# Kernel optimization log

Hardware: AMD Instinct MI355X
Metric: run time of the kernel (lower is better)

Reference implementation:

```python
import jax, jax.numpy as jnp
import numpy as np

# dims
L, D, N, H, FF, F = 2, 512, 8, 64, 2048, 256   # layers, embed, heads, head_dim, ffn, feature_dim
BQ, BC, TQ, TC = 8, 32, 128, 128               # query batch, candidate batch, tokens
EPS = 1e-6


def setup_inputs() -> dict:
    key = jax.random.key(0)
    ks = iter(jax.random.split(key, 64))
    nrm = lambda shape, s=0.02: jax.random.normal(next(ks), shape, jnp.float32) * s
    inp = {
        "c": jax.random.normal(next(ks), (BC, TC, D), jnp.float32),
        "q": jax.random.normal(next(ks), (BQ, TQ, D), jnp.float32),
    }
    for p in ("sa", "ca"):  # self-attn / cross-attn per decoder layer, stacked over L
        inp[f"{p}_wq"] = nrm((L, D, N, H)); inp[f"{p}_bq"] = nrm((L, N, 1, H))
        inp[f"{p}_wk"] = nrm((L, D, N, H)); inp[f"{p}_bk"] = nrm((L, N, 1, H))
        inp[f"{p}_wv"] = nrm((L, D, N, H)); inp[f"{p}_bv"] = nrm((L, N, 1, H))
        inp[f"{p}_wo"] = nrm((L, N, D, H)); inp[f"{p}_bo"] = nrm((L, D))
    for i in (1, 2, 3):  # post-norm LayerNorms
        inp[f"ln{i}_g"] = jnp.ones((L, D), jnp.float32)
        inp[f"ln{i}_b"] = jnp.zeros((L, D), jnp.float32)
    inp["ffn_w1"] = nrm((L, D, FF)); inp["ffn_b1"] = jnp.zeros((L, FF), jnp.float32)
    inp["ffn_w2"] = nrm((L, FF, D)); inp["ffn_b2"] = jnp.zeros((L, D), jnp.float32)
    inp["lnf_g"] = jnp.ones((D,), jnp.float32); inp["lnf_b"] = jnp.zeros((D,), jnp.float32)
    inp["feat_wq"] = nrm((D, F)); inp["feat_bq"] = jnp.zeros((F,), jnp.float32)
    inp["feat_wc"] = nrm((D, F)); inp["feat_bc"] = jnp.zeros((F,), jnp.float32)
    return inp


def _ln(x, g, b):
    m = x.mean(-1, keepdims=True)
    v = ((x - m) ** 2).mean(-1, keepdims=True)
    return (x - m) * jax.lax.rsqrt(v + EPS) * g + b


def _mha4d(xq, xkv, wq, bq, wk, bk, wv, bv, wo, bo):
    # query reads axes as (e,b), key/value as (b,e): the swapped leading axes make
    # the matmul broadcast queries against candidates when e/b are singleton.
    Q = jnp.einsum('ebtd,dnh->ebnth', xq, wq) + bq   # [e,b,n,t,h]
    K = jnp.einsum('betd,dnh->benth', xkv, wk) + bk  # [b,e,n,s,h]
    V = jnp.einsum('betd,dnh->benth', xkv, wv) + bv
    scores = jnp.matmul(Q, jnp.swapaxes(K, -1, -2)) / np.sqrt(H)  # broadcast -> [B,E,n,t,s]
    A = jax.nn.softmax(scores, axis=-1)
    O = jnp.matmul(A, V)                              # [B,E,n,t,h]
    return jnp.einsum('benth,ndh->betd', O, wo) + bo  # [B,E,t,d]


def reference(c, q, sa_wq, sa_bq, sa_wk, sa_bk, sa_wv, sa_bv, sa_wo, sa_bo,
              ca_wq, ca_bq, ca_wk, ca_bk, ca_wv, ca_bv, ca_wo, ca_bo,
              ln1_g, ln1_b, ln2_g, ln2_b, ln3_g, ln3_b,
              ffn_w1, ffn_b1, ffn_w2, ffn_b2, lnf_g, lnf_b,
              feat_wq, feat_bq, feat_wc, feat_bc):
    qm = q[:, None]   # [BQ,1,TQ,D]  encoder memory
    x = c[None]       # [1,BC,TC,D]  decoder input
    for i in range(L):
        a = _mha4d(x, x, sa_wq[i], sa_bq[i], sa_wk[i], sa_bk[i], sa_wv[i], sa_bv[i], sa_wo[i], sa_bo[i])
        x = _ln(x + a, ln1_g[i], ln1_b[i])
        a = _mha4d(x, qm, ca_wq[i], ca_bq[i], ca_wk[i], ca_bk[i], ca_wv[i], ca_bv[i], ca_wo[i], ca_bo[i])
        x = _ln(x + a, ln2_g[i], ln2_b[i])  # x: [BQ,BC,TC,D]
        h = jax.nn.relu(x @ ffn_w1[i] + ffn_b1[i]) @ ffn_w2[i] + ffn_b2[i]
        x = _ln(x + h, ln3_g[i], ln3_b[i])
    x = _ln(x, lnf_g, lnf_b)
    # pooling='avg': drop token 0 then mean over token axis (axis=2)
    qp = qm[:, :, 1:, :].mean(axis=2)  # [BQ,1,D]
    cp = x[:, :, 1:, :].mean(axis=2)   # [BQ,BC,D]
    qf = qp @ feat_wq + feat_bq        # [BQ,1,F]
    cf = cp @ feat_wc + feat_bc        # [BQ,BC,F]
    qn = qf * jax.lax.rsqrt(jnp.maximum((qf ** 2).sum(-1, keepdims=True), 1e-12))
    cn = cf * jax.lax.rsqrt(jnp.maximum((cf ** 2).sum(-1, keepdims=True), 1e-12))
    return (qn * cn).sum(-1)           # [BQ,BC] cosine similarity
```

## Files before the change

kernel.cpp:

```cpp
#include <hip/hip_runtime.h>

using half4  = __attribute__((ext_vector_type(4))) _Float16;
using half8  = __attribute__((ext_vector_type(8))) _Float16;
using floatx4 = __attribute__((ext_vector_type(4))) float;

__device__ __forceinline__ void gl_lds16(const _Float16* g, _Float16* l)
{
  __builtin_amdgcn_global_load_lds(
      (const __attribute__((address_space(1))) void*)g,
      (__attribute__((address_space(3))) void*)l, 16, 0, 0);
}

__global__ __launch_bounds__(256) void gemm_h(
    const _Float16* __restrict__ A, const _Float16* __restrict__ Bt,
    const float* __restrict__ bias, _Float16* __restrict__ C,
    int M, int N, int K, int ldC, int relu)
{
  __shared__ _Float16 As[128 * 32];
  __shared__ _Float16 Bs[128 * 32];
  int tid = threadIdx.x;
  int lane = tid & 63, wave = tid >> 6;
  long bm0 = (long)blockIdx.y * 128;
  int bn0 = blockIdx.x * 128;
  int wm = (wave & 1) * 64, wn = (wave >> 1) * 64;
  int srow = wave * 16 + (lane >> 2);
  int scol = (((lane & 3) ^ ((lane >> 3) & 3)) * 8);
  const _Float16* aA0 = A + (bm0 + srow) * (long)K + scol;
  const _Float16* aA1 = aA0 + 64 * (long)K;
  const _Float16* aB0 = Bt + (bn0 + srow) * (long)K + scol;
  const _Float16* aB1 = aB0 + 64 * (long)K;
  _Float16* lA0 = As + wave * 512;
  _Float16* lA1 = As + 2048 + wave * 512;
  _Float16* lB0 = Bs + wave * 512;
  _Float16* lB1 = Bs + 2048 + wave * 512;
  int mrow = lane & 15, quad = lane >> 4;
  int cofs = (quad ^ ((mrow >> 1) & 3)) * 8;
  floatx4 acc[4][4];
#pragma unroll
  for (int i = 0; i < 4; ++i)
#pragma unroll
    for (int j = 0; j < 4; ++j) acc[i][j] = (floatx4){0.f, 0.f, 0.f, 0.f};

  for (int kt = 0; kt < K; kt += 32) {
    __syncthreads();
    gl_lds16(aA0 + kt, lA0);
    gl_lds16(aA1 + kt, lA1);
    gl_lds16(aB0 + kt, lB0);
    gl_lds16(aB1 + kt, lB1);
    __syncthreads();
    half8 af[4], bf[4];
#pragma unroll
    for (int i = 0; i < 4; ++i)
      af[i] = *(const half8*)&As[(wm + 16 * i + mrow) * 32 + cofs];
#pragma unroll
    for (int j = 0; j < 4; ++j)
      bf[j] = *(const half8*)&Bs[(wn + 16 * j + mrow) * 32 + cofs];
#pragma unroll
    for (int i = 0; i < 4; ++i)
#pragma unroll
      for (int j = 0; j < 4; ++j)
        acc[i][j] = __builtin_amdgcn_mfma_f32_16x16x32_f16(af[i], bf[j], acc[i][j], 0, 0, 0);
  }
#pragma unroll
  for (int j = 0; j < 4; ++j) {
    int n = bn0 + wn + 16 * j + mrow;
    float bj = bias[n];
#pragma unroll
    for (int i = 0; i < 4; ++i) {
#pragma unroll
      for (int r = 0; r < 4; ++r) {
        long m = bm0 + wm + 16 * i + quad * 4 + r;
        float v = acc[i][j][r] + bj;
        if (relu) v = fmaxf(v, 0.f);
        C[m * (long)ldC + n] = (_Float16)v;
      }
    }
  }
}

__global__ __launch_bounds__(256, 2) void gemm_2(
    const _Float16* __restrict__ A, const _Float16* __restrict__ Bt,
    const float* __restrict__ bias, _Float16* __restrict__ C,
    int MT, int NT, int K, int ldC, int relu)
{
  __shared__ _Float16 As[256 * 64];
  __shared__ _Float16 Bs[128 * 64];
  int tid = threadIdx.x;
  int lane = tid & 63, wave = tid >> 6;
  int L = blockIdx.x;
  int xcd = L & 7, seq = L >> 3;
  int band = MT >> 3;
  int mt = xcd * band + seq / NT;
  int nt = seq - (seq / NT) * NT;
  long bm0 = (long)mt * 256;
  int bn0 = nt * 128;
  int r8 = lane >> 3, s8 = lane & 7;
  int scol = (s8 ^ r8) * 8;
  const _Float16* aA = A + (bm0 + wave * 64 + r8) * (long)K + scol;
  const _Float16* aB = Bt + (bn0 + wave * 32 + r8) * (long)K + scol;
  _Float16* lA = As + (wave * 64) * 64;
  _Float16* lB = Bs + (wave * 32) * 64;
  int ll = lane & 15, quad = lane >> 4;
  int lw = ll & 7;
  floatx4 acc[4][8];
#pragma unroll
  for (int i = 0; i < 4; ++i)
#pragma unroll
    for (int j = 0; j < 8; ++j) acc[i][j] = (floatx4){0.f, 0.f, 0.f, 0.f};

  for (int kt = 0; kt < K; kt += 64) {
    __syncthreads();
#pragma unroll
    for (int o = 0; o < 8; ++o)
      gl_lds16(aA + (long)(o * 8) * K + kt, lA + o * 512);
#pragma unroll
    for (int o = 0; o < 4; ++o)
      gl_lds16(aB + (long)(o * 8) * K + kt, lB + o * 512);
    __syncthreads();
#pragma unroll
    for (int k2 = 0; k2 < 2; ++k2) {
      int sofs = ((k2 * 4 + quad) ^ lw) * 8;
      half8 af[4], bf[8];
#pragma unroll
      for (int i = 0; i < 4; ++i)
        af[i] = *(const half8*)&As[(wave * 64 + 16 * i + ll) * 64 + sofs];
#pragma unroll
      for (int j = 0; j < 8; ++j)
        bf[j] = *(const half8*)&Bs[(16 * j + ll) * 64 + sofs];
#pragma unroll
      for (int i = 0; i < 4; ++i)
#pragma unroll
        for (int j = 0; j < 8; ++j)
          acc[i][j] = __builtin_amdgcn_mfma_f32_16x16x32_f16(af[i], bf[j], acc[i][j], 0, 0, 0);
    }
  }
#pragma unroll
  for (int j = 0; j < 8; ++j) {
    int n = bn0 + 16 * j + ll;
    float bj = bias[n];
#pragma unroll
    for (int i = 0; i < 4; ++i) {
#pragma unroll
      for (int r = 0; r < 4; ++r) {
        long m = bm0 + wave * 64 + 16 * i + quad * 4 + r;
        float v = acc[i][j][r] + bj;
        if (relu) v = fmaxf(v, 0.f);
        C[m * (long)ldC + n] = (_Float16)v;
      }
    }
  }
}

__global__ __launch_bounds__(256) void attn_h(
    const _Float16* __restrict__ Qp, int qs,
    const _Float16* __restrict__ Kp, const _Float16* __restrict__ Vp, int ks,
    _Float16* __restrict__ Op, int mode_ca, int l0, int rb0)
{
  __shared__ _Float16 KV[128 * 72];
  __shared__ _Float16 Ps[128 * 136];
  int tid = threadIdx.x;
  int lane = tid & 63, wave = tid >> 6;
  int ll = lane & 15, quad = lane >> 4;
  int idx = blockIdx.x;
  int n = idx & 7;
  int rl = idx >> 3;
  long obase = (long)rl * 128 * 512 + n * 64;
  long qoff, koff;
  if (!mode_ca) {
    qoff = (long)rl * 128 * qs + n * 64;
    koff = (long)rl * 128 * ks + n * 64;
  } else {
    int g = rb0 + rl;
    int a = g >> 5;
    int qblk = l0 ? (g & 31) : rl;
    qoff = (long)qblk * 128 * qs + n * 64;
    koff = (long)a * 128 * ks + n * 64;
  }
#pragma unroll
  for (int it = 0; it < 4; ++it) {
    int e = tid + it * 256;
    int r = e >> 3, c = (e & 7) * 8;
    *(half8*)&KV[r * 72 + c] = *(const half8*)&Kp[koff + (long)r * ks + c];
  }
  half8 aQ[2][2];
#pragma unroll
  for (int i = 0; i < 2; ++i)
#pragma unroll
    for (int k2 = 0; k2 < 2; ++k2)
      aQ[i][k2] = *(const half8*)&Qp[qoff + (long)(wave * 32 + i * 16 + ll) * qs
                                     + quad * 8 + k2 * 32];
  half8 vreg[4];
#pragma unroll
  for (int it = 0; it < 4; ++it) {
    int e = tid + it * 256;
    int vr = e >> 3, c = (e & 7) * 8;
    vreg[it] = *(const half8*)&Vp[koff + (long)vr * ks + c];
  }
  __syncthreads();
  floatx4 accS[2][8];
#pragma unroll
  for (int i = 0; i < 2; ++i)
#pragma unroll
    for (int j = 0; j < 8; ++j) accS[i][j] = (floatx4){0.f, 0.f, 0.f, 0.f};
#pragma unroll
  for (int k2 = 0; k2 < 2; ++k2) {
#pragma unroll
    for (int j = 0; j < 8; ++j) {
      half8 bK = *(const half8*)&KV[(j * 16 + ll) * 72 + quad * 8 + k2 * 32];
      accS[0][j] = __builtin_amdgcn_mfma_f32_16x16x32_f16(aQ[0][k2], bK, accS[0][j], 0, 0, 0);
      accS[1][j] = __builtin_amdgcn_mfma_f32_16x16x32_f16(aQ[1][k2], bK, accS[1][j], 0, 0, 0);
    }
  }
  float rinv[2][4];
#pragma unroll
  for (int i = 0; i < 2; ++i) {
#pragma unroll
    for (int r = 0; r < 4; ++r) {
      float mx = -1e30f;
#pragma unroll
      for (int j = 0; j < 8; ++j) {
        accS[i][j][r] *= 0.125f;
        mx = fmaxf(mx, accS[i][j][r]);
      }
#pragma unroll
      for (int off = 1; off < 16; off <<= 1) mx = fmaxf(mx, __shfl_xor(mx, off));
      float s = 0.f;
#pragma unroll
      for (int j = 0; j < 8; ++j) {
        float e = __expf(accS[i][j][r] - mx);
        accS[i][j][r] = e;
        s += e;
      }
#pragma unroll
      for (int off = 1; off < 16; off <<= 1) s += __shfl_xor(s, off);
      rinv[i][r] = 1.f / s;
      int prow = wave * 32 + i * 16 + quad * 4 + r;
#pragma unroll
      for (int j = 0; j < 8; ++j)
        Ps[prow * 136 + j * 16 + ll] = (_Float16)accS[i][j][r];
    }
  }
  __syncthreads();
#pragma unroll
  for (int it = 0; it < 4; ++it) {
    int e = tid + it * 256;
    int vr = e >> 3, c = (e & 7) * 8;
#pragma unroll
    for (int j = 0; j < 8; ++j) KV[(c + j) * 132 + vr] = vreg[it][j];
  }
  __syncthreads();
  floatx4 accO[2][4];
#pragma unroll
  for (int i = 0; i < 2; ++i)
#pragma unroll
    for (int j = 0; j < 4; ++j) accO[i][j] = (floatx4){0.f, 0.f, 0.f, 0.f};
#pragma unroll
  for (int k4 = 0; k4 < 4; ++k4) {
    half8 aP[2];
#pragma unroll
    for (int i = 0; i < 2; ++i)
      aP[i] = *(const half8*)&Ps[(wave * 32 + i * 16 + ll) * 136 + quad * 8 + k4 * 32];
#pragma unroll
    for (int jh = 0; jh < 4; ++jh) {
      int vb = (jh * 16 + ll) * 132 + quad * 8 + k4 * 32;
      half4 v0 = *(const half4*)&KV[vb];
      half4 v1 = *(const half4*)&KV[vb + 4];
      half8 bV = __builtin_shufflevector(v0, v1, 0, 1, 2, 3, 4, 5, 6, 7);
      accO[0][jh] = __builtin_amdgcn_mfma_f32_16x16x32_f16(aP[0], bV, accO[0][jh], 0, 0, 0);
      accO[1][jh] = __builtin_amdgcn_mfma_f32_16x16x32_f16(aP[1], bV, accO[1][jh], 0, 0, 0);
    }
  }
#pragma unroll
  for (int i = 0; i < 2; ++i)
#pragma unroll
    for (int jh = 0; jh < 4; ++jh)
#pragma unroll
      for (int r = 0; r < 4; ++r) {
        int m = wave * 32 + i * 16 + quad * 4 + r;
        Op[obase + (long)m * 512 + jh * 16 + ll] = (_Float16)(accO[i][jh][r] * rinv[i][r]);
      }
}

__global__ __launch_bounds__(256) void ln_h(
    const void* __restrict__ xin, int xf32, const _Float16* __restrict__ add,
    _Float16* __restrict__ out, const float* __restrict__ g,
    const float* __restrict__ bt, long row0, int bmask)
{
  int rl = blockIdx.x * 4 + (threadIdx.x >> 6);
  long row = row0 + rl;
  int lane = threadIdx.x & 63;
  long xr = (row & (long)bmask) * 512 + lane * 8;
  float v[8];
  if (xf32) {
    float4 a0 = *(const float4*)((const float*)xin + xr);
    float4 a1 = *(const float4*)((const float*)xin + xr + 4);
    v[0] = a0.x; v[1] = a0.y; v[2] = a0.z; v[3] = a0.w;
    v[4] = a1.x; v[5] = a1.y; v[6] = a1.z; v[7] = a1.w;
  } else {
    half8 h = *(const half8*)((const _Float16*)xin + xr);
#pragma unroll
    for (int i = 0; i < 8; ++i) v[i] = (float)h[i];
  }
  if (add) {
    half8 a = *(const half8*)&add[(long)rl * 512 + lane * 8];
#pragma unroll
    for (int i = 0; i < 8; ++i) v[i] += (float)a[i];
  }
  float s = 0.f, sq = 0.f;
#pragma unroll
  for (int i = 0; i < 8; ++i) { s += v[i]; sq += v[i] * v[i]; }
#pragma unroll
  for (int off = 1; off < 64; off <<= 1) {
    s += __shfl_xor(s, off);
    sq += __shfl_xor(sq, off);
  }
  float mean = s * (1.f / 512.f);
  float var = sq * (1.f / 512.f) - mean * mean;
  float rst = rsqrtf(var + 1e-6f);
  int c = lane * 8;
  float4 g0 = *(const float4*)&g[c], g1 = *(const float4*)&g[c + 4];
  float4 b0 = *(const float4*)&bt[c], b1 = *(const float4*)&bt[c + 4];
  float gg[8] = {g0.x, g0.y, g0.z, g0.w, g1.x, g1.y, g1.z, g1.w};
  float bb[8] = {b0.x, b0.y, b0.z, b0.w, b1.x, b1.y, b1.z, b1.w};
  half8 o;
#pragma unroll
  for (int i = 0; i < 8; ++i) o[i] = (_Float16)((v[i] - mean) * rst * gg[i] + bb[i]);
  *(half8*)&out[row * 512 + c] = o;
}

__global__ __launch_bounds__(256) void tconv512(
    const float* __restrict__ w0, const float* __restrict__ w1,
    const float* __restrict__ w2, const float* __restrict__ w3,
    const float* __restrict__ w4, const float* __restrict__ w5,
    _Float16* __restrict__ Wh)
{
  __shared__ float T[64][65];
  int z = blockIdx.z;
  int t = z >> 1, l = z & 1;
  const float* src;
  long off;
  switch (t) {
    case 0: src = w0; off = 0; break;
    case 1: src = w1; off = 262144; break;
    case 2: src = w2; off = 524288; break;
    case 3: src = w3; off = 1048576; break;
    case 4: src = w4; off = 1310720; break;
    default: src = w5; off = 1572864; break;
  }
  src += (long)l * 262144;
  _Float16* out = Wh + (long)l * 4194304 + off;
  int tx = threadIdx.x & 63, tg = threadIdx.x >> 6;
  int r0 = blockIdx.y * 64, c0 = blockIdx.x * 64;
#pragma unroll
  for (int i = 0; i < 16; ++i)
    T[tg + 4 * i][tx] = src[(long)(r0 + tg + 4 * i) * 512 + c0 + tx];
  __syncthreads();
#pragma unroll
  for (int i = 0; i < 16; ++i)
    out[(long)(c0 + tg + 4 * i) * 512 + r0 + tx] = (_Float16)T[tx][tg + 4 * i];
}

__global__ __launch_bounds__(256) void tconvL(const float* __restrict__ in,
                                              _Float16* __restrict__ out, int Rr, int Cc,
                                              long ils, long ols)
{
  __shared__ float T[64][65];
  in += (long)blockIdx.z * ils;
  out += (long)blockIdx.z * ols;
  int tx = threadIdx.x & 63, tg = threadIdx.x >> 6;
  int r0 = blockIdx.y * 64, c0 = blockIdx.x * 64;
#pragma unroll
  for (int i = 0; i < 16; ++i)
    T[tg + 4 * i][tx] = in[(long)(r0 + tg + 4 * i) * Cc + c0 + tx];
  __syncthreads();
#pragma unroll
  for (int i = 0; i < 16; ++i)
    out[(long)(c0 + tg + 4 * i) * Rr + r0 + tx] = (_Float16)T[tx][tg + 4 * i];
}

__global__ void woconvB(const float* __restrict__ sa_wo, const float* __restrict__ ca_wo,
                        _Float16* __restrict__ Wh)
{
  int z = blockIdx.y;
  int s = z >> 1, l = z & 1;
  const float* wo = (s ? ca_wo : sa_wo) + (long)l * 262144;
  _Float16* out = Wh + (long)l * 4194304 + (s ? 1835008 : 786432);
  int o = blockIdx.x * 256 + threadIdx.x;
  int d = o >> 9;
  int nh = o & 511;
  int n = nh >> 6, h = nh & 63;
  out[o] = (_Float16)wo[((long)(n << 9) + d) * 64 + h];
}

__global__ void packbias(const float* __restrict__ sa_bq, const float* __restrict__ sa_bk,
                         const float* __restrict__ sa_bv, const float* __restrict__ ca_bk,
                         const float* __restrict__ ca_bv, float* __restrict__ Bqkv,
                         float* __restrict__ Bkv)
{
  int i = blockIdx.x * 256 + threadIdx.x;
  if (i >= 5120) return;
  int reg = i >> 9, idx = i & 511;
  int l = reg / 5, r = reg % 5;
  int lo = l * 512;
  switch (r) {
    case 0: Bqkv[l * 1536 + idx] = sa_bq[lo + idx]; break;
    case 1: Bqkv[l * 1536 + 512 + idx] = sa_bk[lo + idx]; break;
    case 2: Bqkv[l * 1536 + 1024 + idx] = sa_bv[lo + idx]; break;
    case 3: Bkv[l * 1024 + idx] = ca_bk[lo + idx]; break;
    default: Bkv[l * 1024 + 512 + idx] = ca_bv[lo + idx]; break;
  }
}

__global__ void f2h2(const float* __restrict__ a, _Float16* __restrict__ oa, long na,
                     const float* __restrict__ bsrc, _Float16* __restrict__ ob, long nb)
{
  long i = blockIdx.x * 256L + threadIdx.x;
  if (i < na) oa[i] = (_Float16)a[i];
  else if (i < na + nb) ob[i - na] = (_Float16)bsrc[i - na];
}

__global__ void featq_pool(const float* __restrict__ q, const float* __restrict__ W,
                           const float* __restrict__ bias, float* __restrict__ QN)
{
  __shared__ float sh[512];
  __shared__ float red[256];
  int a = blockIdx.x;
  int f = threadIdx.x;
  for (int dd = f; dd < 512; dd += 256) {
    const float* base = q + (long)a * 65536 + dd;
    float s = 0.f;
    for (int t = 1; t < 128; ++t) s += base[t * 512];
    sh[dd] = s * (1.f / 127.f);
  }
  __syncthreads();
  float acc = bias[f];
  for (int d = 0; d < 512; ++d) acc += sh[d] * W[d * 256 + f];
  red[f] = acc * acc;
  __syncthreads();
  for (int s = 128; s > 0; s >>= 1) {
    if (f < s) red[f] += red[f + s];
    __syncthreads();
  }
  float rn = rsqrtf(fmaxf(red[0], 1e-12f));
  QN[a * 256 + f] = acc * rn;
}

__global__ void featc_pool(const _Float16* __restrict__ X, const float* __restrict__ W,
                           const float* __restrict__ bias, const float* __restrict__ QN,
                           float* __restrict__ out)
{
  __shared__ float sh[512];
  __shared__ float red[256];
  int ab = blockIdx.x;
  int f = threadIdx.x;
  for (int dd = f; dd < 512; dd += 256) {
    const _Float16* base = X + (long)ab * 65536 + dd;
    float s = 0.f;
    for (int t = 1; t < 128; ++t) s += (float)base[t * 512];
    sh[dd] = s * (1.f / 127.f);
  }
  __syncthreads();
  float acc = bias[f];
  for (int d = 0; d < 512; ++d) acc += sh[d] * W[d * 256 + f];
  red[f] = acc * acc;
  __syncthreads();
  for (int s = 128; s > 0; s >>= 1) {
    if (f < s) red[f] += red[f + s];
    __syncthreads();
  }
  float rn = rsqrtf(fmaxf(red[0], 1e-12f));
  float v = acc * rn * QN[(ab >> 5) * 256 + f];
  __syncthreads();
  red[f] = v;
  __syncthreads();
  for (int s = 128; s > 0; s >>= 1) {
    if (f < s) red[f] += red[f + s];
    __syncthreads();
  }
  if (f == 0) out[ab] = red[0];
}

extern "C" void kernel_launch(void* const* d_in, const int* in_sizes, int n_in,
                              void* d_out, int out_size, void* d_ws, size_t ws_size,
                              hipStream_t stream)
{
  (void)in_sizes; (void)n_in; (void)out_size;
  const float* c_in  = (const float*)d_in[0];
  const float* q_in  = (const float*)d_in[1];
  const float* sa_wq = (const float*)d_in[2];
  const float* sa_bq = (const float*)d_in[3];
  const float* sa_wk = (const float*)d_in[4];
  const float* sa_bk = (const float*)d_in[5];
  const float* sa_wv = (const float*)d_in[6];
  const float* sa_bv = (const float*)d_in[7];
  const float* sa_wo = (const float*)d_in[8];
  const float* sa_bo = (const float*)d_in[9];
  const float* ca_wq = (const float*)d_in[10];
  const float* ca_bq = (const float*)d_in[11];
  const float* ca_wk = (const float*)d_in[12];
  const float* ca_bk = (const float*)d_in[13];
  const float* ca_wv = (const float*)d_in[14];
  const float* ca_bv = (const float*)d_in[15];
  const float* ca_wo = (const float*)d_in[16];
  const float* ca_bo = (const float*)d_in[17];
  const float* ln1_g = (const float*)d_in[18];
  const float* ln1_b = (const float*)d_in[19];
  const float* ln2_g = (const float*)d_in[20];
  const float* ln2_b = (const float*)d_in[21];
  const float* ln3_g = (const float*)d_in[22];
  const float* ln3_b = (const float*)d_in[23];
  const float* ffn_w1 = (const float*)d_in[24];
  const float* ffn_b1 = (const float*)d_in[25];
  const float* ffn_w2 = (const float*)d_in[26];
  const float* ffn_b2 = (const float*)d_in[27];
  const float* lnf_g  = (const float*)d_in[28];
  const float* lnf_b  = (const float*)d_in[29];
  const float* feat_wq = (const float*)d_in[30];
  const float* feat_bq = (const float*)d_in[31];
  const float* feat_wc = (const float*)d_in[32];
  const float* feat_bc = (const float*)d_in[33];

  char* p = (char*)d_ws;
  _Float16* Xh  = (_Float16*)p;  p += 33554432;
  _Float16* Xsh = (_Float16*)p;  p += 4194304;
  _Float16* Wh  = (_Float16*)p;  p += 16777216;
  _Float16* qh  = (_Float16*)p;  p += 1048576;
  _Float16* KV0 = (_Float16*)p;  p += 2097152;
  float*    Bqkv = (float*)p;    p += 12288;
  float*    Bkv  = (float*)p;    p += 8192;
  float*    QN  = (float*)p;     p += 8192;
  const size_t fixed_b = (size_t)(p - (char*)d_ws);
  long R = 4096;
  if (ws_size >= fixed_b + 5120UL * 32768) R = 32768;
  else if (ws_size >= fixed_b + 5120UL * 16384) R = 16384;
  else if (ws_size >= fixed_b + 5120UL * 8192) R = 8192;
  _Float16* QKVc = (_Float16*)p; p += R * 3072;
  _Float16* Oc   = (_Float16*)p; p += R * 1024;
  _Float16* Ac   = (_Float16*)p;
  _Float16* Hb = QKVc;
  const int MTR = (int)(R / 256);

  f2h2<<<10240, 256, 0, stream>>>(c_in, Xsh, 2097152, q_in, qh, 524288);
  tconv512<<<dim3(8, 8, 12), 256, 0, stream>>>(sa_wq, sa_wk, sa_wv, ca_wq, ca_wk, ca_wv, Wh);
  woconvB<<<dim3(1024, 4), 256, 0, stream>>>(sa_wo, ca_wo, Wh);
  tconvL<<<dim3(32, 8, 2), 256, 0, stream>>>(ffn_w1, Wh + 2097152, 512, 2048, 1048576, 4194304);
  tconvL<<<dim3(8, 32, 2), 256, 0, stream>>>(ffn_w2, Wh + 3145728, 2048, 512, 1048576, 4194304);
  packbias<<<20, 256, 0, stream>>>(sa_bq, sa_bk, sa_bv, ca_bk, ca_bv, Bqkv, Bkv);

  {
    _Float16* Wl = Wh;
    gemm_h<<<dim3(12, 32), 256, 0, stream>>>(Xsh, Wl + 0, Bqkv, QKVc, 4096, 1536, 512, 1536, 0);
    attn_h<<<256, 256, 0, stream>>>(QKVc, 1536, QKVc + 512, QKVc + 1024, 1536, Oc, 0, 0, 0);
    gemm_h<<<dim3(4, 32), 256, 0, stream>>>(Oc, Wl + 786432, sa_bo, Ac, 4096, 512, 512, 512, 0);
    ln_h<<<1024, 256, 0, stream>>>(c_in, 1, Ac, Xsh, ln1_g, ln1_b, 0, 0x7FFFFFFF);
    gemm_h<<<dim3(4, 32), 256, 0, stream>>>(Xsh, Wl + 1048576, ca_bq, QKVc, 4096, 512, 512, 1536, 0);
    gemm_h<<<dim3(8, 8), 256, 0, stream>>>(qh, Wl + 1310720, Bkv, KV0, 1024, 1024, 512, 1024, 0);
    for (long c = 0; c < 32768; c += R) {
      attn_h<<<(R / 128) * 8, 256, 0, stream>>>(QKVc, 1536, KV0, KV0 + 512, 1024, Oc,
                                                1, 1, (int)(c / 128));
      gemm_2<<<MTR * 4, 256, 0, stream>>>(Oc, Wl + 1835008, ca_bo, Ac, MTR, 4, 512, 512, 0);
      ln_h<<<R / 4, 256, 0, stream>>>(Xsh, 0, Ac, Xh, ln2_g, ln2_b, c, 4095);
      gemm_2<<<MTR * 16, 256, 0, stream>>>(Xh + c * 512, Wl + 2097152,
                                           ffn_b1, Hb, MTR, 16, 512, 2048, 1);
      gemm_2<<<MTR * 4, 256, 0, stream>>>(Hb, Wl + 3145728, ffn_b2, Ac, MTR, 4, 2048, 512, 0);
      ln_h<<<R / 4, 256, 0, stream>>>(Xh, 0, Ac, Xh, ln3_g, ln3_b, c, 0x7FFFFFFF);
    }
  }
  {
    _Float16* Wl = Wh + 4194304;
    gemm_h<<<dim3(8, 8), 256, 0, stream>>>(qh, Wl + 1310720, Bkv + 1024, KV0, 1024, 1024, 512, 1024, 0);
    for (long c = 0; c < 32768; c += R) {
      _Float16* Xhc = Xh + c * 512;
      gemm_2<<<MTR * 12, 256, 0, stream>>>(Xhc, Wl + 0, Bqkv + 1536, QKVc, MTR, 12, 512, 1536, 0);
      attn_h<<<(R / 128) * 8, 256, 0, stream>>>(QKVc, 1536, QKVc + 512, QKVc + 1024, 1536,
                                                Oc, 0, 0, 0);
      gemm_2<<<MTR * 4, 256, 0, stream>>>(Oc, Wl + 786432, sa_bo + 512, Ac, MTR, 4, 512, 512, 0);
      ln_h<<<R / 4, 256, 0, stream>>>(Xh, 0, Ac, Xh, ln1_g + 512, ln1_b + 512, c, 0x7FFFFFFF);
      gemm_2<<<MTR * 4, 256, 0, stream>>>(Xhc, Wl + 1048576, ca_bq + 512, QKVc, MTR, 4, 512, 1536, 0);
      attn_h<<<(R / 128) * 8, 256, 0, stream>>>(QKVc, 1536, KV0, KV0 + 512, 1024, Oc,
                                                1, 0, (int)(c / 128));
      gemm_2<<<MTR * 4, 256, 0, stream>>>(Oc, Wl + 1835008, ca_bo + 512, Ac, MTR, 4, 512, 512, 0);
      ln_h<<<R / 4, 256, 0, stream>>>(Xh, 0, Ac, Xh, ln2_g + 512, ln2_b + 512, c, 0x7FFFFFFF);
      gemm_2<<<MTR * 16, 256, 0, stream>>>(Xh + c * 512, Wl + 2097152,
                                           ffn_b1 + 2048, Hb, MTR, 16, 512, 2048, 1);
      gemm_2<<<MTR * 4, 256, 0, stream>>>(Hb, Wl + 3145728, ffn_b2 + 512, Ac, MTR, 4, 2048, 512, 0);
      ln_h<<<R / 4, 256, 0, stream>>>(Xh, 0, Ac, Xh, ln3_g + 512, ln3_b + 512, c, 0x7FFFFFFF);
    }
  }
  ln_h<<<8192, 256, 0, stream>>>(Xh, 0, nullptr, Xh, lnf_g, lnf_b, 0, 0x7FFFFFFF);
  featq_pool<<<8, 256, 0, stream>>>(q_in, feat_wq, feat_bq, QN);
  featc_pool<<<256, 256, 0, stream>>>(Xh, feat_wc, feat_bc, QN, (float*)d_out);
}
```

Baseline: 925.7 us.

## Replace 256x128 gemm_2 with 128x128 gemm_h and fuse final LayerNorm

Removes the larger-tile gemm_2 kernel (256x128 tiles, K-step 64, XCD-aware block mapping) and routes every chunked GEMM through the 128x128 gemm_h kernel. Separately, the final LayerNorm is folded into the last layer's ln3 launch through an optional second gamma/beta pair, which drops one full pass over the activations. The smaller tiles give more blocks per launch but lower data reuse per block and lose the XCD-aware scheduling.

Result: slower. 1.156 ms (+24.9%).

```diff
diff --git a/kernel.cpp b/kernel.cpp
--- a/kernel.cpp
+++ b/kernel.cpp
@@ -78,79 +78,6 @@
   }
 }
 
-__global__ __launch_bounds__(256, 2) void gemm_2(
-    const _Float16* __restrict__ A, const _Float16* __restrict__ Bt,
-    const float* __restrict__ bias, _Float16* __restrict__ C,
-    int MT, int NT, int K, int ldC, int relu)
-{
-  __shared__ _Float16 As[256 * 64];
-  __shared__ _Float16 Bs[128 * 64];
-  int tid = threadIdx.x;
-  int lane = tid & 63, wave = tid >> 6;
-  int L = blockIdx.x;
-  int xcd = L & 7, seq = L >> 3;
-  int band = MT >> 3;
-  int mt = xcd * band + seq / NT;
-  int nt = seq - (seq / NT) * NT;
-  long bm0 = (long)mt * 256;
-  int bn0 = nt * 128;
-  int r8 = lane >> 3, s8 = lane & 7;
-  int scol = (s8 ^ r8) * 8;
-  const _Float16* aA = A + (bm0 + wave * 64 + r8) * (long)K + scol;
-  const _Float16* aB = Bt + (bn0 + wave * 32 + r8) * (long)K + scol;
-  _Float16* lA = As + (wave * 64) * 64;
-  _Float16* lB = Bs + (wave * 32) * 64;
-  int ll = lane & 15, quad = lane >> 4;
-  int lw = ll & 7;
-  floatx4 acc[4][8];
-#pragma unroll
-  for (int i = 0; i < 4; ++i)
-#pragma unroll
-    for (int j = 0; j < 8; ++j) acc[i][j] = (floatx4){0.f, 0.f, 0.f, 0.f};
-
-  for (int kt = 0; kt < K; kt += 64) {
-    __syncthreads();
-#pragma unroll
-    for (int o = 0; o < 8; ++o)
-      gl_lds16(aA + (long)(o * 8) * K + kt, lA + o * 512);
-#pragma unroll
-    for (int o = 0; o < 4; ++o)
-      gl_lds16(aB + (long)(o * 8) * K + kt, lB + o * 512);
-    __syncthreads();
-#pragma unroll
-    for (int k2 = 0; k2 < 2; ++k2) {
-      int sofs = ((k2 * 4 + quad) ^ lw) * 8;
-      half8 af[4], bf[8];
-#pragma unroll
-      for (int i = 0; i < 4; ++i)
-        af[i] = *(const half8*)&As[(wave * 64 + 16 * i + ll) * 64 + sofs];
-#pragma unroll
-      for (int j = 0; j < 8; ++j)
-        bf[j] = *(const half8*)&Bs[(16 * j + ll) * 64 + sofs];
-#pragma unroll
-      for (int i = 0; i < 4; ++i)
-#pragma unroll
-        for (int j = 0; j < 8; ++j)
-          acc[i][j] = __builtin_amdgcn_mfma_f32_16x16x32_f16(af[i], bf[j], acc[i][j], 0, 0, 0);
-    }
-  }
-#pragma unroll
-  for (int j = 0; j < 8; ++j) {
-    int n = bn0 + 16 * j + ll;
-    float bj = bias[n];
-#pragma unroll
-    for (int i = 0; i < 4; ++i) {
-#pragma unroll
-      for (int r = 0; r < 4; ++r) {
-        long m = bm0 + wave * 64 + 16 * i + quad * 4 + r;
-        float v = acc[i][j][r] + bj;
-        if (relu) v = fmaxf(v, 0.f);
-        C[m * (long)ldC + n] = (_Float16)v;
-      }
-    }
-  }
-}
-
 __global__ __launch_bounds__(256) void attn_h(
     const _Float16* __restrict__ Qp, int qs,
     const _Float16* __restrict__ Kp, const _Float16* __restrict__ Vp, int ks,
@@ -284,7 +211,8 @@
 __global__ __launch_bounds__(256) void ln_h(
     const void* __restrict__ xin, int xf32, const _Float16* __restrict__ add,
     _Float16* __restrict__ out, const float* __restrict__ g,
-    const float* __restrict__ bt, long row0, int bmask)
+    const float* __restrict__ bt, long row0, int bmask,
+    const float* __restrict__ g2, const float* __restrict__ bt2)
 {
   int rl = blockIdx.x * 4 + (threadIdx.x >> 6);
   long row = row0 + rl;
@@ -322,9 +250,30 @@
   float4 b0 = *(const float4*)&bt[c], b1 = *(const float4*)&bt[c + 4];
   float gg[8] = {g0.x, g0.y, g0.z, g0.w, g1.x, g1.y, g1.z, g1.w};
   float bb[8] = {b0.x, b0.y, b0.z, b0.w, b1.x, b1.y, b1.z, b1.w};
+#pragma unroll
+  for (int i = 0; i < 8; ++i) v[i] = (v[i] - mean) * rst * gg[i] + bb[i];
+  if (g2) {
+    float s2 = 0.f, sq2 = 0.f;
+#pragma unroll
+    for (int i = 0; i < 8; ++i) { s2 += v[i]; sq2 += v[i] * v[i]; }
+#pragma unroll
+    for (int off = 1; off < 64; off <<= 1) {
+      s2 += __shfl_xor(s2, off);
+      sq2 += __shfl_xor(sq2, off);
+    }
+    float mean2 = s2 * (1.f / 512.f);
+    float var2 = sq2 * (1.f / 512.f) - mean2 * mean2;
+    float rst2 = rsqrtf(var2 + 1e-6f);
+    float4 e0 = *(const float4*)&g2[c], e1 = *(const float4*)&g2[c + 4];
+    float4 f0 = *(const float4*)&bt2[c], f1 = *(const float4*)&bt2[c + 4];
+    float ee[8] = {e0.x, e0.y, e0.z, e0.w, e1.x, e1.y, e1.z, e1.w};
+    float ff[8] = {f0.x, f0.y, f0.z, f0.w, f1.x, f1.y, f1.z, f1.w};
+#pragma unroll
+    for (int i = 0; i < 8; ++i) v[i] = (v[i] - mean2) * rst2 * ee[i] + ff[i];
+  }
   half8 o;
 #pragma unroll
-  for (int i = 0; i < 8; ++i) o[i] = (_Float16)((v[i] - mean) * rst * gg[i] + bb[i]);
+  for (int i = 0; i < 8; ++i) o[i] = (_Float16)v[i];
   *(half8*)&out[row * 512 + c] = o;
 }
 
@@ -538,7 +487,7 @@
   _Float16* Oc   = (_Float16*)p; p += R * 1024;
   _Float16* Ac   = (_Float16*)p;
   _Float16* Hb = QKVc;
-  const int MTR = (int)(R / 256);
+  const int MR = (int)(R / 128);
 
   f2h2<<<10240, 256, 0, stream>>>(c_in, Xsh, 2097152, q_in, qh, 524288);
   tconv512<<<dim3(8, 8, 12), 256, 0, stream>>>(sa_wq, sa_wk, sa_wv, ca_wq, ca_wk, ca_wv, Wh);
@@ -552,18 +501,23 @@
     gemm_h<<<dim3(12, 32), 256, 0, stream>>>(Xsh, Wl + 0, Bqkv, QKVc, 4096, 1536, 512, 1536, 0);
     attn_h<<<256, 256, 0, stream>>>(QKVc, 1536, QKVc + 512, QKVc + 1024, 1536, Oc, 0, 0, 0);
     gemm_h<<<dim3(4, 32), 256, 0, stream>>>(Oc, Wl + 786432, sa_bo, Ac, 4096, 512, 512, 512, 0);
-    ln_h<<<1024, 256, 0, stream>>>(c_in, 1, Ac, Xsh, ln1_g, ln1_b, 0, 0x7FFFFFFF);
+    ln_h<<<1024, 256, 0, stream>>>(c_in, 1, Ac, Xsh, ln1_g, ln1_b, 0, 0x7FFFFFFF,
+                                   nullptr, nullptr);
     gemm_h<<<dim3(4, 32), 256, 0, stream>>>(Xsh, Wl + 1048576, ca_bq, QKVc, 4096, 512, 512, 1536, 0);
     gemm_h<<<dim3(8, 8), 256, 0, stream>>>(qh, Wl + 1310720, Bkv, KV0, 1024, 1024, 512, 1024, 0);
     for (long c = 0; c < 32768; c += R) {
       attn_h<<<(R / 128) * 8, 256, 0, stream>>>(QKVc, 1536, KV0, KV0 + 512, 1024, Oc,
                                                 1, 1, (int)(c / 128));
-      gemm_2<<<MTR * 4, 256, 0, stream>>>(Oc, Wl + 1835008, ca_bo, Ac, MTR, 4, 512, 512, 0);
-      ln_h<<<R / 4, 256, 0, stream>>>(Xsh, 0, Ac, Xh, ln2_g, ln2_b, c, 4095);
-      gemm_2<<<MTR * 16, 256, 0, stream>>>(Xh + c * 512, Wl + 2097152,
-                                           ffn_b1, Hb, MTR, 16, 512, 2048, 1);
-      gemm_2<<<MTR * 4, 256, 0, stream>>>(Hb, Wl + 3145728, ffn_b2, Ac, MTR, 4, 2048, 512, 0);
-      ln_h<<<R / 4, 256, 0, stream>>>(Xh, 0, Ac, Xh, ln3_g, ln3_b, c, 0x7FFFFFFF);
+      gemm_h<<<dim3(4, MR), 256, 0, stream>>>(Oc, Wl + 1835008, ca_bo, Ac,
+                                              (int)R, 512, 512, 512, 0);
+      ln_h<<<R / 4, 256, 0, stream>>>(Xsh, 0, Ac, Xh, ln2_g, ln2_b, c, 4095,
+                                      nullptr, nullptr);
+      gemm_h<<<dim3(16, MR), 256, 0, stream>>>(Xh + c * 512, Wl + 2097152,
+                                               ffn_b1, Hb, (int)R, 2048, 512, 2048, 1);
+      gemm_h<<<dim3(4, MR), 256, 0, stream>>>(Hb, Wl + 3145728, ffn_b2, Ac,
+                                              (int)R, 512, 2048, 512, 0);
+      ln_h<<<R / 4, 256, 0, stream>>>(Xh, 0, Ac, Xh, ln3_g, ln3_b, c, 0x7FFFFFFF,
+                                      nullptr, nullptr);
     }
   }
   {
@@ -571,23 +525,30 @@
     gemm_h<<<dim3(8, 8), 256, 0, stream>>>(qh, Wl + 1310720, Bkv + 1024, KV0, 1024, 1024, 512, 1024, 0);
     for (long c = 0; c < 32768; c += R) {
       _Float16* Xhc = Xh + c * 512;
-      gemm_2<<<MTR * 12, 256, 0, stream>>>(Xhc, Wl + 0, Bqkv + 1536, QKVc, MTR, 12, 512, 1536, 0);
+      gemm_h<<<dim3(12, MR), 256, 0, stream>>>(Xhc, Wl + 0, Bqkv + 1536, QKVc,
+                                               (int)R, 1536, 512, 1536, 0);
       attn_h<<<(R / 128) * 8, 256, 0, stream>>>(QKVc, 1536, QKVc + 512, QKVc + 1024, 1536,
                                                 Oc, 0, 0, 0);
-      gemm_2<<<MTR * 4, 256, 0, stream>>>(Oc, Wl + 786432, sa_bo + 512, Ac, MTR, 4, 512, 512, 0);
-      ln_h<<<R / 4, 256, 0, stream>>>(Xh, 0, Ac, Xh, ln1_g + 512, ln1_b + 512, c, 0x7FFFFFFF);
-      gemm_2<<<MTR * 4, 256, 0, stream>>>(Xhc, Wl + 1048576, ca_bq + 512, QKVc, MTR, 4, 512, 1536, 0);
+      gemm_h<<<dim3(4, MR), 256, 0, stream>>>(Oc, Wl + 786432, sa_bo + 512, Ac,
+                                              (int)R, 512, 512, 512, 0);
+      ln_h<<<R / 4, 256, 0, stream>>>(Xh, 0, Ac, Xh, ln1_g + 512, ln1_b + 512, c, 0x7FFFFFFF,
+                                      nullptr, nullptr);
+      gemm_h<<<dim3(4, MR), 256, 0, stream>>>(Xhc, Wl + 1048576, ca_bq + 512, QKVc,
+                                              (int)R, 512, 512, 1536, 0);
       attn_h<<<(R / 128) * 8, 256, 0, stream>>>(QKVc, 1536, KV0, KV0 + 512, 1024, Oc,
                                                 1, 0, (int)(c / 128));
-      gemm_2<<<MTR * 4, 256, 0, stream>>>(Oc, Wl + 1835008, ca_bo + 512, Ac, MTR, 4, 512, 512, 0);
-      ln_h<<<R / 4, 256, 0, stream>>>(Xh, 0, Ac, Xh, ln2_g + 512, ln2_b + 512, c, 0x7FFFFFFF);
-      gemm_2<<<MTR * 16, 256, 0, stream>>>(Xh + c * 512, Wl + 2097152,
-                                           ffn_b1 + 2048, Hb, MTR, 16, 512, 2048, 1);
-      gemm_2<<<MTR * 4, 256, 0, stream>>>(Hb, Wl + 3145728, ffn_b2 + 512, Ac, MTR, 4, 2048, 512, 0);
-      ln_h<<<R / 4, 256, 0, stream>>>(Xh, 0, Ac, Xh, ln3_g + 512, ln3_b + 512, c, 0x7FFFFFFF);
-    }
-  }
-  ln_h<<<8192, 256, 0, stream>>>(Xh, 0, nullptr, Xh, lnf_g, lnf_b, 0, 0x7FFFFFFF);
+      gemm_h<<<dim3(4, MR), 256, 0, stream>>>(Oc, Wl + 1835008, ca_bo + 512, Ac,
+                                              (int)R, 512, 512, 512, 0);
+      ln_h<<<R / 4, 256, 0, stream>>>(Xh, 0, Ac, Xh, ln2_g + 512, ln2_b + 512, c, 0x7FFFFFFF,
+                                      nullptr, nullptr);
+      gemm_h<<<dim3(16, MR), 256, 0, stream>>>(Xh + c * 512, Wl + 2097152,
+                                               ffn_b1 + 2048, Hb, (int)R, 2048, 512, 2048, 1);
+      gemm_h<<<dim3(4, MR), 256, 0, stream>>>(Hb, Wl + 3145728, ffn_b2 + 512, Ac,
+                                              (int)R, 512, 2048, 512, 0);
+      ln_h<<<R / 4, 256, 0, stream>>>(Xh, 0, Ac, Xh, ln3_g + 512, ln3_b + 512, c, 0x7FFFFFFF,
+                                      lnf_g, lnf_b);
+    }
+  }
   featq_pool<<<8, 256, 0, stream>>>(q_in, feat_wq, feat_bq, QN);
   featc_pool<<<256, 256, 0, stream>>>(Xh, feat_wc, feat_bc, QN, (float*)d_out);
 }
```
